# Optimization experiments

Measured on AMD Instinct MI355X. Metric: run time of the kernel, lower is better.

The kernel has to match this reference:

```python
import jax, jax.numpy as jnp
import numpy as np

H = 16  # hidden_size
NUM_MLP = 8   # relu, tanh, elu, silu, gelu, none, selu, softplus
NUM_EXPERTS = 12  # 8 MLPs + abs, modulus, sin, cos


def setup_inputs() -> dict:
    key = jax.random.key(0)
    ks = jax.random.split(key, 6)
    B, S, C = 16, 2048, 16
    x = jax.random.normal(ks[0], (B, S, C, 2), dtype=jnp.float32)
    # Stacked per-expert MLP params: Linear(3 -> H) then Linear(H -> 1).
    # (Torch init zeroes the last layer; we use random weights to exercise the math.)
    W1 = jax.random.normal(ks[1], (NUM_MLP, 3, H), dtype=jnp.float32) * (1.0 / np.sqrt(3.0))
    b1 = jax.random.normal(ks[2], (NUM_MLP, H), dtype=jnp.float32) * 0.02
    W2 = jax.random.normal(ks[3], (NUM_MLP, H, 1), dtype=jnp.float32) * (1.0 / np.sqrt(H))
    b2 = jax.random.normal(ks[4], (NUM_MLP, 1), dtype=jnp.float32) * 0.02
    expert_weights = jnp.full((NUM_EXPERTS,), 1.0 / NUM_EXPERTS, dtype=jnp.float32)
    return {"x": x, "W1": W1, "b1": b1, "W2": W2, "b2": b2,
            "expert_weights": expert_weights}


_ACTS = [
    jax.nn.relu,
    jnp.tanh,
    jax.nn.elu,
    jax.nn.silu,
    lambda v: jax.nn.gelu(v, approximate=False),  # torch nn.GELU default = exact
    lambda v: v,                                   # 'none'
    jax.nn.selu,
    jax.nn.softplus,
]


def reference(x, W1, b1, W2, b2, expert_weights):
    # x: (B, S, C, 2) -> output (B, S, C, 1, 1)
    re, im = x[..., 0], x[..., 1]
    amp = jnp.sqrt(re * re + im * im)            # torch.norm over last dim
    feats = jnp.stack([re, im, amp], axis=-1)    # (B,S,C,3)

    outs = []
    for i, act in enumerate(_ACTS):
        h = act(feats @ W1[i] + b1[i])           # (B,S,C,H)
        outs.append(h @ W2[i] + b2[i])           # (B,S,C,1)

    outs.append((jnp.abs(re) + jnp.abs(im))[..., None])  # 'abs'
    outs.append(amp[..., None])                           # 'modulus'
    outs.append(jnp.sin(amp)[..., None])                  # 'sin'
    outs.append(jnp.cos(amp)[..., None])                  # 'cos'

    expert_outputs = jnp.stack(outs, axis=-1)    # (B,S,C,1,12)
    return jnp.sum(expert_outputs * expert_weights, axis=-1, keepdims=True)  # (B,S,C,1,1)
```

## Files before the change

### kernel.cpp

```cpp
#include <hip/hip_runtime.h>

constexpr int BLK = 256;
constexpr int P   = 2;

__device__ __forceinline__ float fast_rcp(float x) { return __builtin_amdgcn_rcpf(x); }

template<int A> __device__ __forceinline__ float act_fn(float x);
template<> __device__ __forceinline__ float act_fn<0>(float x) { return fmaxf(x, 0.0f); }
template<> __device__ __forceinline__ float act_fn<1>(float x) {
    float e = __expf(2.0f * x);
    return fmaf(-2.0f, fast_rcp(1.0f + e), 1.0f);
}
template<> __device__ __forceinline__ float act_fn<2>(float x) {
    return x > 0.0f ? x : (__expf(x) - 1.0f);
}
template<> __device__ __forceinline__ float act_fn<3>(float x) {
    return x * fast_rcp(1.0f + __expf(-x));
}
template<> __device__ __forceinline__ float act_fn<4>(float x) {
    return x * fast_rcp(1.0f + __expf(-1.702f * x));
}
template<> __device__ __forceinline__ float act_fn<5>(float x) { return x; }
template<> __device__ __forceinline__ float act_fn<6>(float x) {
    const float sc   = 1.0507009873554805f;
    const float scal = 1.7580993408473766f;
    float n = fmaf(scal, __expf(x), -scal);
    return x > 0.0f ? sc * x : n;
}
template<> __device__ __forceinline__ float act_fn<7>(float x) {
    return fmaxf(x, 0.0f) + __logf(1.0f + __expf(-fabsf(x)));
}

template<int A>
__device__ __forceinline__ void run_expert(const float* __restrict__ W1,
                                           const float* __restrict__ b1,
                                           const float* __restrict__ W2,
                                           const float* __restrict__ ew,
                                           const float* re, const float* im,
                                           const float* am, float* acc) {
    float accE[P];
#pragma unroll
    for (int k = 0; k < P; ++k) accE[k] = 0.0f;

#pragma unroll
    for (int h = 0; h < 16; ++h) {
        const float wre = W1[A * 48 + h];
        const float wim = W1[A * 48 + 16 + h];
        const float wam = W1[A * 48 + 32 + h];
        const float bb  = b1[A * 16 + h];
        const float w2  = W2[A * 16 + h];
#pragma unroll
        for (int k = 0; k < P; ++k) {
            float z = fmaf(re[k], wre, fmaf(im[k], wim, fmaf(am[k], wam, bb)));
            accE[k] = fmaf(act_fn<A>(z), w2, accE[k]);
        }
    }
    const float ewI = ew[A];
#pragma unroll
    for (int k = 0; k < P; ++k) acc[k] = fmaf(accE[k], ewI, acc[k]);
    __builtin_amdgcn_sched_barrier(0);
}

__global__ __launch_bounds__(BLK, 4)
void moe_kernel(const float* __restrict__ x,
                const float* __restrict__ W1,
                const float* __restrict__ b1,
                const float* __restrict__ W2,
                const float* __restrict__ b2,
                const float* __restrict__ ew,
                float* __restrict__ out, int npts) {
    const int p0 = blockIdx.x * (BLK * P) + threadIdx.x * P;
    if (p0 >= npts) return;

    float bconst = 0.0f;
#pragma unroll
    for (int i = 0; i < 8; ++i) bconst = fmaf(ew[i], b2[i], bconst);
    const float ewA = ew[8], ewM = ew[9], ewS = ew[10], ewC = ew[11];

    float4 v = reinterpret_cast<const float4*>(x)[p0 >> 1];
    float re[P] = {v.x, v.z};
    float im[P] = {v.y, v.w};
    float am[P], acc[P];

#pragma unroll
    for (int k = 0; k < P; ++k) {
        am[k] = __builtin_amdgcn_sqrtf(fmaf(re[k], re[k], im[k] * im[k]));
        float a = fmaf(ewA, fabsf(re[k]) + fabsf(im[k]), bconst);
        a = fmaf(ewM, am[k], a);
        a = fmaf(ewS, __sinf(am[k]), a);
        a = fmaf(ewC, __cosf(am[k]), a);
        acc[k] = a;
    }

    run_expert<0>(W1, b1, W2, ew, re, im, am, acc);
    run_expert<1>(W1, b1, W2, ew, re, im, am, acc);
    run_expert<2>(W1, b1, W2, ew, re, im, am, acc);
    run_expert<3>(W1, b1, W2, ew, re, im, am, acc);
    run_expert<4>(W1, b1, W2, ew, re, im, am, acc);
    run_expert<5>(W1, b1, W2, ew, re, im, am, acc);
    run_expert<6>(W1, b1, W2, ew, re, im, am, acc);
    run_expert<7>(W1, b1, W2, ew, re, im, am, acc);

    reinterpret_cast<float2*>(out)[p0 >> 1] = make_float2(acc[0], acc[1]);
}

extern "C" void kernel_launch(void* const* d_in, const int* in_sizes, int n_in,
                              void* d_out, int out_size, void* d_ws, size_t ws_size,
                              hipStream_t stream) {
    const float* x  = (const float*)d_in[0];
    const float* W1 = (const float*)d_in[1];
    const float* b1 = (const float*)d_in[2];
    const float* W2 = (const float*)d_in[3];
    const float* b2 = (const float*)d_in[4];
    const float* ew = (const float*)d_in[5];
    float* out = (float*)d_out;

    const int npts = in_sizes[0] / 2;
    const int blocks = (npts + BLK * P - 1) / (BLK * P);
    hipLaunchKernelGGL(moe_kernel, dim3(blocks), dim3(BLK), 0, stream,
                       x, W1, b1, W2, b2, ew, out, npts);
}
```

Measured before the change: 24.05 us.

## Use one point per thread, exp2/hardware sin-cos, and branchless activation math

Each thread now handles one point instead of two, and the occupancy hint in launch bounds rises from 4 to 8 blocks. Activations call the hardware exp2 builtin with LOG2E-prescaled arguments and use branchless max/min forms, and softplus replaces the log call with a polynomial in 1+exp(-|z|). Sin and cos use the hardware builtins on am/2pi, which avoids range reduction. The aim is fewer transcendental instructions and better latency hiding from more waves. In exchange the softplus polynomial approximation may lose accuracy, and per-thread work and instruction-level parallelism drop.

```diff
diff --git a/kernel.cpp b/kernel.cpp
--- a/kernel.cpp
+++ b/kernel.cpp
@@ -1,34 +1,55 @@
 #include <hip/hip_runtime.h>
 
 constexpr int BLK = 256;
-constexpr int P   = 2;
 
 __device__ __forceinline__ float fast_rcp(float x) { return __builtin_amdgcn_rcpf(x); }
 
-template<int A> __device__ __forceinline__ float act_fn(float x);
-template<> __device__ __forceinline__ float act_fn<0>(float x) { return fmaxf(x, 0.0f); }
-template<> __device__ __forceinline__ float act_fn<1>(float x) {
-    float e = __expf(2.0f * x);
-    return fmaf(-2.0f, fast_rcp(1.0f + e), 1.0f);
+__device__ __forceinline__ float fast_exp2(float x) {
+#if __has_builtin(__builtin_amdgcn_exp2f)
+    return __builtin_amdgcn_exp2f(x);
+#else
+    return __expf(x * 0.6931471805599453f);
+#endif
 }
-template<> __device__ __forceinline__ float act_fn<2>(float x) {
-    return x > 0.0f ? x : (__expf(x) - 1.0f);
+
+#define LOG2E 1.4426950408889634f
+
+__device__ __forceinline__ float max0(float x) { return fmaxf(x, 0.0f); }
+__device__ __forceinline__ float min0(float x) { return fminf(x, 0.0f); }
+
+template<int A> __device__ __forceinline__ float act_fn(float z);
+template<> __device__ __forceinline__ float act_fn<0>(float z) { return max0(z); }
+template<> __device__ __forceinline__ float act_fn<1>(float z) {
+    float e = fast_exp2(z * (2.0f * LOG2E));
+    return fmaf(-2.0f, fast_rcp(e + 1.0f), 1.0f);
 }
-template<> __device__ __forceinline__ float act_fn<3>(float x) {
-    return x * fast_rcp(1.0f + __expf(-x));
+template<> __device__ __forceinline__ float act_fn<2>(float z) {
+    float em = fast_exp2(z * LOG2E) - 1.0f;
+    return max0(z) + min0(em);
 }
-template<> __device__ __forceinline__ float act_fn<4>(float x) {
-    return x * fast_rcp(1.0f + __expf(-1.702f * x));
+template<> __device__ __forceinline__ float act_fn<3>(float z) {
+    float d = fast_exp2(z * (-LOG2E)) + 1.0f;
+    return z * fast_rcp(d);
 }
-template<> __device__ __forceinline__ float act_fn<5>(float x) { return x; }
-template<> __device__ __forceinline__ float act_fn<6>(float x) {
+template<> __device__ __forceinline__ float act_fn<4>(float z) {
+    float d = fast_exp2(z * (-1.702f * LOG2E)) + 1.0f;
+    return z * fast_rcp(d);
+}
+template<> __device__ __forceinline__ float act_fn<5>(float z) { return z; }
+template<> __device__ __forceinline__ float act_fn<6>(float z) {
     const float sc   = 1.0507009873554805f;
     const float scal = 1.7580993408473766f;
-    float n = fmaf(scal, __expf(x), -scal);
-    return x > 0.0f ? sc * x : n;
+    float e = fast_exp2(z * LOG2E);
+    float n = fmaf(scal, e, -scal);
+    return fmaf(max0(z), sc, min0(n));
 }
-template<> __device__ __forceinline__ float act_fn<7>(float x) {
-    return fmaxf(x, 0.0f) + __logf(1.0f + __expf(-fabsf(x)));
+template<> __device__ __forceinline__ float act_fn<7>(float z) {
+    float m = fast_exp2(fabsf(z) * (-LOG2E)) + 1.0f;
+    float p = fmaf(-0.056570851f, m, 0.44717955f);
+    p = fmaf(p, m, -1.4699568f);
+    p = fmaf(p, m, 2.8212026f);
+    p = fmaf(p, m, -1.7417939f);
+    return max0(z) + p;
 }
 
 template<int A>
@@ -36,12 +57,8 @@
                                            const float* __restrict__ b1,
                                            const float* __restrict__ W2,
                                            const float* __restrict__ ew,
-                                           const float* re, const float* im,
-                                           const float* am, float* acc) {
-    float accE[P];
-#pragma unroll
-    for (int k = 0; k < P; ++k) accE[k] = 0.0f;
-
+                                           float re, float im, float am, float& acc) {
+    float accE = 0.0f;
 #pragma unroll
     for (int h = 0; h < 16; ++h) {
         const float wre = W1[A * 48 + h];
@@ -49,19 +66,14 @@
         const float wam = W1[A * 48 + 32 + h];
         const float bb  = b1[A * 16 + h];
         const float w2  = W2[A * 16 + h];
-#pragma unroll
-        for (int k = 0; k < P; ++k) {
-            float z = fmaf(re[k], wre, fmaf(im[k], wim, fmaf(am[k], wam, bb)));
-            accE[k] = fmaf(act_fn<A>(z), w2, accE[k]);
-        }
+        float z = fmaf(re, wre, fmaf(im, wim, fmaf(am, wam, bb)));
+        accE = fmaf(act_fn<A>(z), w2, accE);
     }
-    const float ewI = ew[A];
-#pragma unroll
-    for (int k = 0; k < P; ++k) acc[k] = fmaf(accE[k], ewI, acc[k]);
+    acc = fmaf(accE, ew[A], acc);
     __builtin_amdgcn_sched_barrier(0);
 }
 
-__global__ __launch_bounds__(BLK, 4)
+__global__ __launch_bounds__(BLK, 8)
 void moe_kernel(const float* __restrict__ x,
                 const float* __restrict__ W1,
                 const float* __restrict__ b1,
@@ -69,28 +81,26 @@
                 const float* __restrict__ b2,
                 const float* __restrict__ ew,
                 float* __restrict__ out, int npts) {
-    const int p0 = blockIdx.x * (BLK * P) + threadIdx.x * P;
-    if (p0 >= npts) return;
+    const int p = blockIdx.x * BLK + threadIdx.x;
+    if (p >= npts) return;
 
     float bconst = 0.0f;
 #pragma unroll
     for (int i = 0; i < 8; ++i) bconst = fmaf(ew[i], b2[i], bconst);
-    const float ewA = ew[8], ewM = ew[9], ewS = ew[10], ewC = ew[11];
 
-    float4 v = reinterpret_cast<const float4*>(x)[p0 >> 1];
-    float re[P] = {v.x, v.z};
-    float im[P] = {v.y, v.w};
-    float am[P], acc[P];
+    float2 v = reinterpret_cast<const float2*>(x)[p];
+    const float re = v.x, im = v.y;
+    const float am = __builtin_amdgcn_sqrtf(fmaf(re, re, im * im));
 
-#pragma unroll
-    for (int k = 0; k < P; ++k) {
-        am[k] = __builtin_amdgcn_sqrtf(fmaf(re[k], re[k], im[k] * im[k]));
-        float a = fmaf(ewA, fabsf(re[k]) + fabsf(im[k]), bconst);
-        a = fmaf(ewM, am[k], a);
-        a = fmaf(ewS, __sinf(am[k]), a);
-        a = fmaf(ewC, __cosf(am[k]), a);
-        acc[k] = a;
-    }
+    const float INV2PI = 0.15915494309189535f;
+    const float s  = am * INV2PI;
+    const float sn = __builtin_amdgcn_sinf(s);
+    const float cs = __builtin_amdgcn_cosf(s);
+
+    float acc = fmaf(ew[8], fabsf(re) + fabsf(im), bconst);
+    acc = fmaf(ew[9],  am, acc);
+    acc = fmaf(ew[10], sn, acc);
+    acc = fmaf(ew[11], cs, acc);
 
     run_expert<0>(W1, b1, W2, ew, re, im, am, acc);
     run_expert<1>(W1, b1, W2, ew, re, im, am, acc);
@@ -101,7 +111,7 @@
     run_expert<6>(W1, b1, W2, ew, re, im, am, acc);
     run_expert<7>(W1, b1, W2, ew, re, im, am, acc);
 
-    reinterpret_cast<float2*>(out)[p0 >> 1] = make_float2(acc[0], acc[1]);
+    out[p] = acc;
 }
 
 extern "C" void kernel_launch(void* const* d_in, const int* in_sizes, int n_in,
@@ -116,7 +126,7 @@
     float* out = (float*)d_out;
 
     const int npts = in_sizes[0] / 2;
-    const int blocks = (npts + BLK * P - 1) / (BLK * P);
+    const int blocks = (npts + BLK - 1) / BLK;
     hipLaunchKernelGGL(moe_kernel, dim3(blocks), dim3(BLK), 0, stream,
                        x, W1, b1, W2, b2, ew, out, npts);
 }
```

Result: no change. 24.44 us (+1.6%).
